# Optimization experiments

Hardware: AMD Instinct MI355X
Metric: run time of the kernel (lower is better)

Reference implementation:

```python
import jax, jax.numpy as jnp
import numpy as np

N, P = 25000, 400000          # atoms, pairs
F, E, EH = 64, 32, 64         # nr_atom_basis, nr_edge_basis, nr_edge_basis_hidden
FH, SSH, S = 64, 64, 64       # node hidden, spatial hidden, spatial
FV, C, H, K = 64, 32, 4, 50   # velocity hidden, coefficients, heads, rbf
R_MAX = 0.5                   # maximum_interaction_radius (nm)
EPS = 1e-8
SCALE = 1.0                   # scale_factor_in_nanometer


def physnet_rbf(d):
    # PhysNet RBF: exp(-beta * (exp(-d) - mu_k)^2), mu_k in [exp(-r_max), 1]
    mu = jnp.linspace(np.exp(-R_MAX), 1.0, K).astype(jnp.float32)
    beta = jnp.float32(((2.0 / K) * (1.0 - np.exp(-R_MAX))) ** -2)
    return jnp.exp(-beta * (jnp.exp(-d)[:, None] - mu) ** 2)  # [P, K]


def seg_sum(v, idx, n):
    return jax.ops.segment_sum(v, idx, num_segments=n)


def seg_mean(v, idx, n):
    # matches torch scatter_reduce 'mean' with include_self=False (empty segments -> 0)
    s = seg_sum(v, idx, n)
    cnt = seg_sum(jnp.ones((v.shape[0],), v.dtype), idx, n)
    cnt = jnp.maximum(cnt, 1.0).reshape((n,) + (1,) * (v.ndim - 1))
    return s / cnt


def seg_softmax(a, idx, n):
    # numerically-stable per-receiver softmax over variable neighbor sets
    m = jax.ops.segment_max(a, idx, num_segments=n)
    m = jnp.where(jnp.isfinite(m), m, 0.0)
    e = jnp.exp(a - m[idx])
    return e / seg_sum(e, idx, n)[idx]


def setup_inputs():
    key = jax.random.key(0)
    ks = jax.random.split(key, 20)
    def w(k, shape):
        return jax.random.normal(k, shape, jnp.float32) * 0.05
    z = lambda *s: jnp.zeros(s, jnp.float32)
    return dict(
        h=jax.random.normal(ks[0], (N, F), jnp.float32),
        x=jax.random.uniform(ks[1], (N, 3), jnp.float32),
        v=jax.random.normal(ks[2], (N, 3), jnp.float32) * 0.1,
        idx_i=jax.random.randint(ks[3], (P,), 0, N),
        idx_j=jax.random.randint(ks[4], (P,), 0, N),
        W_ein=w(ks[5], (2 * F, K)), b_ein=z(K),
        W_eo1=w(ks[6], (2 * F + K + 1, EH)), b_eo1=z(EH),
        W_eo2=w(ks[7], (EH, E)), b_eo2=z(E),
        W_att=w(ks[8], (E, H)), b_att=z(H),
        W_xm=w(ks[9], (H * E, C)),
        W_vm=w(ks[10], (C,)),
        W_pn1=w(ks[11], (C, SSH)), b_pn1=z(SSH),
        W_pn2=w(ks[12], (SSH, S)), b_pn2=z(S),
        W_n1=w(ks[13], (F + H * E + S, FH)), b_n1=z(FH),
        W_n2=w(ks[14], (FH, F)), b_n2=z(F),
        W_v1=w(ks[15], (F, FV)), b_v1=z(FV),
        W_v2=w(ks[16], (FV, 1)),
    )


def reference(h, x, v, idx_i, idx_j,
              W_ein, b_ein, W_eo1, b_eo1, W_eo2, b_eo2,
              W_att, b_att, W_xm, W_vm,
              W_pn1, b_pn1, W_pn2, b_pn2,
              W_n1, b_n1, W_n2, b_n2,
              W_v1, b_v1, W_v2):
    act = jax.nn.silu
    # geometry
    r_ij = x[idx_j] - x[idx_i]                       # [P, 3]
    d_ij = jnp.sqrt(jnp.sum(r_ij ** 2, axis=-1) + EPS)
    dir_ij = r_ij / (d_ij[:, None] + EPS)
    # edge update (Eq. 7): RBF-filtered edge MLP
    h_cat = jnp.concatenate([h[idx_i], h[idx_j]], axis=-1)          # [P, 2F]
    filtered = physnet_rbf(d_ij) * (h_cat @ W_ein + b_ein)          # [P, K]
    edge_in = jnp.concatenate([h_cat, filtered, (d_ij / SCALE)[:, None]], axis=-1)
    h_ij_edge = act(edge_in @ W_eo1 + b_eo1) @ W_eo2 + b_eo2        # [P, E]
    # multi-head semantic attention: segment softmax per receiver
    att = jax.nn.celu(h_ij_edge @ W_att + b_att, alpha=2.0)         # [P, H]
    att_w = seg_softmax(att, idx_i, N)                              # [P, H]
    h_ij_sem = (h_ij_edge[:, :, None] * att_w[:, None, :]).reshape(P, E * H)
    # neighborhood aggregation
    h_i_sem = seg_sum(h_ij_sem, idx_i, N)                           # [N, E*H]
    # spatial attention (Eq. 6)
    comb = jnp.tanh(h_ij_sem @ W_xm)[:, :, None] * dir_ij[:, None, :]  # [P, C, 3]
    comb_mean = seg_mean(comb, idx_i, N)                            # [N, C, 3]
    comb_norm2 = jnp.sum(comb_mean ** 2, axis=-1)                   # [N, C]
    h_i_spatial = act(act(comb_norm2 @ W_pn1 + b_pn1) @ W_pn2 + b_pn2)
    # node update (Eq. 4)
    node_in = jnp.concatenate([h, h_i_sem, h_i_spatial], axis=-1)
    h_new = h + act(act(node_in @ W_n1 + b_n1) @ W_n2 + b_n2)
    # velocity update (Eq. 12)
    v_ij = jnp.einsum('pcx,c->px', comb, W_vm)                      # [P, 3]
    dv = seg_mean(v_ij, idx_i, N)                                   # [N, 3]
    gate = 2.0 * jax.nn.sigmoid(act(h_new @ W_v1 + b_v1) @ W_v2)    # [N, 1]
    v_new = gate * v + dv
    x_new = x + v_new
    return h_new, x_new, v_new
```

## Files before the change

kernel.cpp:

```cpp
#include <hip/hip_runtime.h>
#include <hip/hip_bf16.h>

#define DEV __device__ __forceinline__

constexpr int N_ = 25000;
constexpr int P_ = 400000;

constexpr int align4(int xx){ return (xx+3)&~3; }
constexpr int OFF_CNT     = 0;
constexpr int OFF_OFFSETS = align4(OFF_CNT + N_);
constexpr int OFF_CURSOR  = align4(OFF_OFFSETS + N_ + 1);
constexpr int OFF_EDGE    = align4(OFF_CURSOR + N_);
constexpr int OFF_E4      = OFF_EDGE + P_*16;
constexpr int OFF_DIR     = OFF_E4 + P_*4;
constexpr int OFF_SEM     = align4(OFF_DIR + P_*4);
constexpr int OFF_N2      = OFF_SEM + N_*64;
constexpr int OFF_DV      = OFF_N2 + N_*16;
constexpr int OFF_WB5     = OFF_DV + N_*4;
constexpr int OFF_WB6     = OFF_WB5 + 1024;
constexpr int OFF_WB7     = OFF_WB6 + 2048;
constexpr int OFF_WB8     = OFF_WB7 + 8192;
constexpr int OFF_WB9     = OFF_WB8 + 2048;
constexpr int OFF_HB      = OFF_WB9 + 2048;
constexpr int OFF_SIJ     = OFF_HB + N_*32;
constexpr int OFF_WB1     = OFF_SIJ + P_*2;
constexpr int OFF_WB2     = OFF_WB1 + 8192;
constexpr int OFF_WB3     = OFF_WB2 + 2048;
constexpr int OFF_WB4     = OFF_WB3 + 1024;
constexpr int OFF_RANK    = OFF_WB4 + 2048;
constexpr int WS_UNITS    = OFF_RANK + P_;

constexpr float MU0F  = 0.60653065971263342f;
constexpr float DMUF  = (1.0f - 0.60653065971263342f) / 49.0f;
constexpr float BETAF = 1.0f / ((0.04f * (1.0f - 0.60653065971263342f)) *
                                (0.04f * (1.0f - 0.60653065971263342f)));
constexpr float EPSF  = 1e-8f;

DEV float u2f(unsigned int u){ union{unsigned int i; float f;} c; c.i=u; return c.f; }
DEV unsigned int f2b16(float f){
  __hip_bfloat16 b = __float2bfloat16(f);
  unsigned short s; __builtin_memcpy(&s, &b, 2);
  return (unsigned int)s;
}
DEV unsigned int pack2(float a, float b){ return f2b16(a) | (f2b16(b) << 16); }
DEV float frcp(float x){ return __builtin_amdgcn_rcpf(x); }
DEV float silu_f(float v){ return v * frcp(1.0f + __expf(-v)); }

using short8 = __attribute__((ext_vector_type(8))) short;
using f32x4  = __attribute__((ext_vector_type(4))) float;
union U4S8 { uint4 u; short8 s; };
DEV short8 ld_frag(const void* p){ U4S8 c; c.u = *(const uint4*)p; return c.s; }
DEV f32x4 mfma16(short8 a, short8 b, f32x4 c){
  return __builtin_amdgcn_mfma_f32_16x16x32_bf16(a, b, c, 0, 0, 0);
}

__global__ void k_hist(const int* __restrict__ idx_i,
                       int* __restrict__ cnt, int* __restrict__ rank){
  int t = blockIdx.x*256 + threadIdx.x;
  if (t < P_) rank[t] = atomicAdd(&cnt[idx_i[t]], 1);
}

__global__ __launch_bounds__(1024) void k_scan2(
    const int* __restrict__ cnt, int* __restrict__ offsets,
    const float* __restrict__ h,
    const float* __restrict__ Wein, const float* __restrict__ Weo1,
    const float* __restrict__ Weo2, const float* __restrict__ Wxm,
    const float* __restrict__ Wpn1, const float* __restrict__ Wpn2,
    const float* __restrict__ Wn1,  const float* __restrict__ Wn2,
    const float* __restrict__ Wv1,
    unsigned int* __restrict__ hb,
    unsigned short* __restrict__ wb1, unsigned short* __restrict__ wb2,
    unsigned short* __restrict__ wb3, unsigned short* __restrict__ wb4,
    unsigned short* __restrict__ wb5, unsigned short* __restrict__ wb6,
    unsigned short* __restrict__ wb7, unsigned short* __restrict__ wb8,
    unsigned short* __restrict__ wb9){
  __shared__ unsigned short sCnt[N_];
  __shared__ int swv[16];
  if (blockIdx.x == 0){
    const int t = threadIdx.x;
    const int wv = t >> 6, ln = t & 63;
    for (int q = t; q < N_; q += 1024) sCnt[q] = (unsigned short)cnt[q];
    __syncthreads();
    constexpr int CH = (N_ + 1023)/1024;
    int b = t*CH, e = b+CH;
    if (b > N_) b = N_;
    if (e > N_) e = N_;
    int s = 0;
    for (int q=b; q<e; q++) s += sCnt[q];
    int incl = s;
    #pragma unroll
    for (int off=1; off<64; off<<=1){
      int vv = __shfl_up(incl, off);
      if (ln >= off) incl += vv;
    }
    if (ln == 63) swv[wv] = incl;
    __syncthreads();
    if (wv == 0 && ln < 16){
      int w = swv[ln];
      #pragma unroll
      for (int off=1; off<16; off<<=1){
        int vv = __shfl_up(w, off);
        if (ln >= off) w += vv;
      }
      swv[ln] = w;
    }
    __syncthreads();
    const int wpre = (wv > 0) ? swv[wv-1] : 0;
    int run = wpre + incl - s;
    for (int q=b; q<e; q++){ offsets[q] = run; run += sCnt[q]; }
    if (t == 1023) offsets[N_] = run;
    return;
  }
  int t = (blockIdx.x-1)*1024 + threadIdx.x;
  const int st = (gridDim.x-1)*1024;
  for (int q=t; q<N_*32; q+=st){
    float2 a = *(const float2*)(h + (size_t)q*2);
    hb[q] = pack2(a.x, a.y);
  }
  for (int q=t; q<8*4*64*8; q+=st){
    int e=q&7, lane=(q>>3)&63, sx=(q>>9)&3, nf=q>>11;
    int l15=lane&15, quad=lane>>4;
    int n = 16*nf + l15, k = sx*32 + quad*8 + e;
    float v = (n<50) ? Wein[k*50+n] : ((n<64) ? 0.f : Weo1[k*64+(n-64)]);
    wb1[q] = (unsigned short)f2b16(v);
  }
  for (int q=t; q<4*2*64*8; q+=st){
    int e=q&7, lane=(q>>3)&63, sx=(q>>9)&1, nf=q>>10;
    int l15=lane&15, quad=lane>>4;
    int n = 16*nf + l15, k = sx*32 + quad*8 + e;
    float v = (k<50) ? Weo1[(128+k)*64+n] : ((k==50) ? Weo1[178*64+n] : 0.f);
    wb2[q] = (unsigned short)f2b16(v);
  }
  for (int q=t; q<2*2*64*8; q+=st){
    int e=q&7, lane=(q>>3)&63, sx=(q>>9)&1, nf=q>>10;
    int l15=lane&15, quad=lane>>4;
    int n = 16*nf + l15, k = sx*32 + quad*8 + e;
    wb3[q] = (unsigned short)f2b16(Weo2[k*32+n]);
  }
  for (int q=t; q<8*64*8; q+=st){
    int e=q&7, lane=(q>>3)&63, nf=q>>9;
    int l15=lane&15, quad=lane>>4;
    int k = quad*8 + e;
    int n_log = l15*8 + nf;
    int cc = n_log>>2, hh = n_log&3;
    wb4[q] = (unsigned short)f2b16(Wxm[(k*4+hh)*32 + cc]);
  }
  for (int q=t; q<4*64*8; q+=st){
    int e=q&7, lane=(q>>3)&63, nf=q>>9;
    int l15=lane&15, quad=lane>>4;
    int n = 16*nf + l15, k = quad*8 + e;
    wb5[q] = (unsigned short)f2b16(Wpn1[k*64+n]);
  }
  for (int q=t; q<4*2*64*8; q+=st){
    int e=q&7, lane=(q>>3)&63, sx=(q>>9)&1, nf=q>>10;
    int l15=lane&15, quad=lane>>4;
    int n = 16*nf + l15, k = sx*32 + quad*8 + e;
    wb6[q] = (unsigned short)f2b16(Wpn2[k*64+n]);
    wb8[q] = (unsigned short)f2b16(Wn2[k*64+n]);
    wb9[q] = (unsigned short)f2b16(Wv1[k*64+n]);
  }
  for (int q=t; q<4*8*64*8; q+=st){
    int e=q&7, lane=(q>>3)&63, sx=(q>>9)&7, nf=q>>12;
    int l15=lane&15, quad=lane>>4;
    int n = 16*nf + l15, k = sx*32 + quad*8 + e;
    wb7[q] = (unsigned short)f2b16(Wn1[k*64+n]);
  }
}

__global__ void k_scatter3(const int* __restrict__ idx_i, const int* __restrict__ idx_j,
                           const int* __restrict__ offsets, const int* __restrict__ rank,
                           int* __restrict__ sij){
  int t = blockIdx.x*256 + threadIdx.x;
  if (t >= P_) return;
  int i = idx_i[t], j = idx_j[t];
  int pos = offsets[i] + rank[t];
  *(int2*)(sij + (size_t)pos*2) = make_int2(i, j);
}

__global__ __launch_bounds__(256, 4) void k_edge2(
    const unsigned short* __restrict__ hb,
    const int* __restrict__ sij, const float* __restrict__ x,
    float* __restrict__ dir4,
    const unsigned short* __restrict__ wb1, const unsigned short* __restrict__ wb2,
    const unsigned short* __restrict__ wb3,
    const float* __restrict__ bein, const float* __restrict__ beo1,
    const float* __restrict__ beo2, const float* __restrict__ Watt,
    const float* __restrict__ batt,
    unsigned int* __restrict__ edge_out, float* __restrict__ e4_out)
{
  __shared__ __align__(16) unsigned char sAll[4*4608];
  __shared__ float sdv[128];
  __shared__ float semd[128];

  const int tid  = threadIdx.x;
  const int wv   = tid >> 6;
  const int lane = tid & 63;
  const int l15  = lane & 15;
  const int quad = lane >> 4;
  const int pbase = blockIdx.x * 128;
  unsigned char* sW = sAll + wv*4608;

  if (lane < 32){
    int row = 32*wv + lane;
    int2 ij = *(const int2*)(sij + (size_t)(pbase + row)*2);
    float xi0=x[ij.x*3], xi1=x[ij.x*3+1], xi2=x[ij.x*3+2];
    float xj0=x[ij.y*3], xj1=x[ij.y*3+1], xj2=x[ij.y*3+2];
    float rx=xj0-xi0, ry=xj1-xi1, rz=xj2-xi2;
    float d = sqrtf(rx*rx+ry*ry+rz*rz+EPSF);
    float iv = frcp(d+EPSF);
    sdv[row]  = d;
    semd[row] = __expf(-d);
    *(float4*)(dir4 + (size_t)(pbase + row)*4) = make_float4(rx*iv, ry*iv, rz*iv, d);
  }

  short8 af0[4], af1[4];
  {
    const int rbase = pbase + 32*wv;
    int2 ij0 = *(const int2*)(sij + (size_t)(rbase + l15)*2);
    int2 ij1 = *(const int2*)(sij + (size_t)(rbase + 16 + l15)*2);
    const unsigned char* hB = (const unsigned char*)hb;
    af0[0] = ld_frag(hB + (size_t)ij0.x*128 + quad*16);
    af0[1] = ld_frag(hB + (size_t)ij0.x*128 + 64 + quad*16);
    af0[2] = ld_frag(hB + (size_t)ij0.y*128 + quad*16);
    af0[3] = ld_frag(hB + (size_t)ij0.y*128 + 64 + quad*16);
    af1[0] = ld_frag(hB + (size_t)ij1.x*128 + quad*16);
    af1[1] = ld_frag(hB + (size_t)ij1.x*128 + 64 + quad*16);
    af1[2] = ld_frag(hB + (size_t)ij1.y*128 + quad*16);
    af1[3] = ld_frag(hB + (size_t)ij1.y*128 + 64 + quad*16);
  }

  f32x4 acc[2][4];
  #pragma unroll
  for (int mf=0; mf<2; mf++)
    #pragma unroll
    for (int nf=0; nf<4; nf++){
      int nn = 16*nf + l15;
      float bias = (nn < 50) ? bein[nn] : 0.f;
      acc[mf][nf] = (f32x4){bias, bias, bias, bias};
    }
  #pragma unroll
  for (int s=0; s<4; s++){
    #pragma unroll
    for (int nf=0; nf<4; nf++){
      short8 b = ld_frag((const unsigned char*)wb1 + (size_t)((nf*4 + s)*64 + lane)*16);
      acc[0][nf] = mfma16(af0[s], b, acc[0][nf]);
      acc[1][nf] = mfma16(af1[s], b, acc[1][nf]);
    }
  }

  #pragma unroll
  for (int mf=0; mf<2; mf++)
    #pragma unroll
    for (int nf=0; nf<4; nf++){
      int n = 16*nf + l15;
      float mu = MU0F + (float)n*DMUF;
      #pragma unroll
      for (int reg=0; reg<4; reg++){
        int lrow = 16*mf + quad*4 + reg;
        int grow = 32*wv + lrow;
        float t = semd[grow] - mu;
        float fv = acc[mf][nf][reg] * __expf(-BETAF*t*t);
        unsigned short ob;
        if (n < 50)       ob = (unsigned short)f2b16(fv);
        else if (n == 50) ob = (unsigned short)f2b16(sdv[grow]);
        else              ob = 0;
        ((unsigned short*)sW)[lrow*72 + n] = ob;
      }
    }

  #pragma unroll
  for (int mf=0; mf<2; mf++)
    #pragma unroll
    for (int nf=0; nf<4; nf++){
      float bias = beo1[16*nf + l15];
      acc[mf][nf] = (f32x4){bias, bias, bias, bias};
    }
  #pragma unroll
  for (int s=0; s<4; s++){
    #pragma unroll
    for (int nf=0; nf<4; nf++){
      short8 b = ld_frag((const unsigned char*)wb1 + (size_t)(((4+nf)*4 + s)*64 + lane)*16);
      acc[0][nf] = mfma16(af0[s], b, acc[0][nf]);
      acc[1][nf] = mfma16(af1[s], b, acc[1][nf]);
    }
  }

  #pragma unroll
  for (int s=0; s<2; s++){
    int koff = s*32 + quad*8;
    short8 a0 = ld_frag(sW + l15*144      + koff*2);
    short8 a1 = ld_frag(sW + (16+l15)*144 + koff*2);
    #pragma unroll
    for (int nf=0; nf<4; nf++){
      short8 b = ld_frag((const unsigned char*)wb2 + (size_t)((nf*2 + s)*64 + lane)*16);
      acc[0][nf] = mfma16(a0, b, acc[0][nf]);
      acc[1][nf] = mfma16(a1, b, acc[1][nf]);
    }
  }

  unsigned char* A3 = sW;
  #pragma unroll
  for (int mf=0; mf<2; mf++)
    #pragma unroll
    for (int nf=0; nf<4; nf++){
      int n = 16*nf + l15;
      #pragma unroll
      for (int reg=0; reg<4; reg++){
        int lrow = 16*mf + quad*4 + reg;
        ((unsigned short*)A3)[lrow*72 + n] = (unsigned short)f2b16(silu_f(acc[mf][nf][reg]));
      }
    }

  f32x4 acc3[2][2];
  #pragma unroll
  for (int mf=0; mf<2; mf++)
    #pragma unroll
    for (int nf=0; nf<2; nf++){
      float bias = beo2[16*nf + l15];
      acc3[mf][nf] = (f32x4){bias, bias, bias, bias};
    }
  #pragma unroll
  for (int s=0; s<2; s++){
    int koff = s*32 + quad*8;
    short8 a0 = ld_frag(A3 + l15*144      + koff*2);
    short8 a1 = ld_frag(A3 + (16+l15)*144 + koff*2);
    #pragma unroll
    for (int nf=0; nf<2; nf++){
      short8 b = ld_frag((const unsigned char*)wb3 + (size_t)((nf*2 + s)*64 + lane)*16);
      acc3[0][nf] = mfma16(a0, b, acc3[0][nf]);
      acc3[1][nf] = mfma16(a1, b, acc3[1][nf]);
    }
  }

  #pragma unroll
  for (int mf=0; mf<2; mf++)
    #pragma unroll
    for (int nf=0; nf<2; nf++){
      int n = 16*nf + l15;
      #pragma unroll
      for (int reg=0; reg<4; reg++){
        int lrow = 16*mf + quad*4 + reg;
        ((float*)sW)[lrow*36 + n] = acc3[mf][nf][reg];
      }
    }

  {
    int rr = lane >> 1;
    int p = pbase + 32*wv + rr;
    int cb = (lane & 1) * 16;
    const float* er = (const float*)(sW + rr*144);
    float l0, l1, l2, l3;
    if ((lane & 1) == 0){ l0 = batt[0]; l1 = batt[1]; l2 = batt[2]; l3 = batt[3]; }
    else                { l0 = l1 = l2 = l3 = 0.f; }
    float ecache[16];
    {
      float4 v0 = *(const float4*)(er + cb);
      float4 v1 = *(const float4*)(er + cb + 4);
      float4 v2 = *(const float4*)(er + cb + 8);
      float4 v3 = *(const float4*)(er + cb + 12);
      ecache[0]=v0.x; ecache[1]=v0.y; ecache[2]=v0.z; ecache[3]=v0.w;
      ecache[4]=v1.x; ecache[5]=v1.y; ecache[6]=v1.z; ecache[7]=v1.w;
      ecache[8]=v2.x; ecache[9]=v2.y; ecache[10]=v2.z; ecache[11]=v2.w;
      ecache[12]=v3.x; ecache[13]=v3.y; ecache[14]=v3.z; ecache[15]=v3.w;
    }
    #pragma unroll
    for (int c=0;c<16;c++){
      float ev = ecache[c];
      const float4 wr = *(const float4*)(Watt + (cb + c)*4);
      l0 += ev*wr.x; l1 += ev*wr.y; l2 += ev*wr.z; l3 += ev*wr.w;
    }
    l0 += __shfl_xor(l0,1); l1 += __shfl_xor(l1,1);
    l2 += __shfl_xor(l2,1); l3 += __shfl_xor(l3,1);
    if ((lane & 1) == 0){
      float e0 = __expf(l0 > 0.f ? l0 : 2.f*(__expf(l0*0.5f)-1.f));
      float e1 = __expf(l1 > 0.f ? l1 : 2.f*(__expf(l1*0.5f)-1.f));
      float e2 = __expf(l2 > 0.f ? l2 : 2.f*(__expf(l2*0.5f)-1.f));
      float e3 = __expf(l3 > 0.f ? l3 : 2.f*(__expf(l3*0.5f)-1.f));
      *(float4*)(e4_out + (size_t)p*4) = make_float4(e0, e1, e2, e3);
    }
    uint4 o1 = make_uint4(pack2(ecache[0],ecache[1]),  pack2(ecache[2],ecache[3]),
                          pack2(ecache[4],ecache[5]),  pack2(ecache[6],ecache[7]));
    uint4 o2 = make_uint4(pack2(ecache[8],ecache[9]),  pack2(ecache[10],ecache[11]),
                          pack2(ecache[12],ecache[13]),pack2(ecache[14],ecache[15]));
    unsigned int* ep = edge_out + (size_t)p*16 + (lane&1)*8;
    *(uint4*)(ep)     = o1;
    *(uint4*)(ep + 4) = o2;
  }
}

__global__ __launch_bounds__(256, 4) void k_agg(
    const int* __restrict__ offsets,
    const unsigned int* __restrict__ edgeb,
    const float* __restrict__ e4,
    const float* __restrict__ dir4,
    const unsigned short* __restrict__ wb4,
    const float* __restrict__ Wvm,
    unsigned int* __restrict__ semB, unsigned int* __restrict__ n2B,
    float* __restrict__ wsDv)
{
  __shared__ __align__(16) unsigned char sAllB[4*5632];
  const int wv   = threadIdx.x >> 6;
  const int lane = threadIdx.x & 63;
  unsigned char* sA = sAllB + wv*5632;
  unsigned char* gC = sA + 1024;
  float* sE = (float*)(sA + 5120);
  float* sD = (float*)(sA + 5376);

  const int c    = lane & 31;
  const int l15  = lane & 15;
  const int quad = lane >> 4;
  const int half = lane >> 5;
  const bool low = (lane < 32);

  short8 b4[8];
  #pragma unroll
  for (int nf=0; nf<8; nf++)
    b4[nf] = ld_frag((const unsigned char*)wb4 + (size_t)(nf*64 + lane)*16);
  const float wvm_c = Wvm[c];

  const int i = blockIdx.x*4 + wv;
  if (i >= N_) return;
  const int n0 = offsets[i], n1 = offsets[i+1];
  const int cnt = n1 - n0;

  {
    const int nc0 = min(16, cnt);
    if (lane < 32){
      if (lane*32 < nc0*64){
        const uint4* src = (const uint4*)(edgeb + (size_t)n0*16 + lane*8);
        *(uint4*)(sA + lane*32)      = src[0];
        *(uint4*)(sA + lane*32 + 16) = src[1];
      }
    } else if (lane < 48){
      int k = lane - 32;
      if (k < nc0) *(float4*)(sE + k*4) = *(const float4*)(e4 + (size_t)(n0+k)*4);
    } else {
      int k = lane - 48;
      if (k < nc0) *(float4*)(sD + k*4) = *(const float4*)(dir4 + (size_t)(n0+k)*4);
    }
  }

  float d0=0.f,d1=0.f,d2=0.f,d3=0.f;
  for (int s = n0 + lane; s < n1; s += 64){
    const float4 ev = *(const float4*)(e4 + (size_t)s*4);
    d0+=ev.x; d1+=ev.y; d2+=ev.z; d3+=ev.w;
  }
  #pragma unroll
  for (int off=32; off>=1; off>>=1){
    d0 += __shfl_xor(d0,off); d1 += __shfl_xor(d1,off);
    d2 += __shfl_xor(d2,off); d3 += __shfl_xor(d3,off);
  }
  const float i0 = (cnt>0)?frcp(d0):0.f, i1 = (cnt>0)?frcp(d1):0.f;
  const float i2 = (cnt>0)?frcp(d2):0.f, i3 = (cnt>0)?frcp(d3):0.f;

  float sem4[4] = {0.f,0.f,0.f,0.f};
  float cx=0.f,cy=0.f,cz=0.f, gx=0.f,gy=0.f,gz=0.f;

  bool staged = true;
  for (int base = n0; base < n1; base += 16){
    const int nc = min(16, n1 - base);
    if (!staged){
      if (lane < 32){
        if (lane*32 < nc*64){
          const uint4* src = (const uint4*)(edgeb + (size_t)base*16 + lane*8);
          *(uint4*)(sA + lane*32)      = src[0];
          *(uint4*)(sA + lane*32 + 16) = src[1];
        }
      } else if (lane < 48){
        int k = lane - 32;
        if (k < nc) *(float4*)(sE + k*4) = *(const float4*)(e4 + (size_t)(base+k)*4);
      } else {
        int k = lane - 48;
        if (k < nc) *(float4*)(sD + k*4) = *(const float4*)(dir4 + (size_t)(base+k)*4);
      }
    }
    staged = false;
    {
      short8 a0 = ld_frag(sA + l15*64 + quad*16);
      f32x4 accg[8];
      #pragma unroll
      for (int nf=0; nf<8; nf++){
        f32x4 z = (f32x4){0.f,0.f,0.f,0.f};
        accg[nf] = mfma16(a0, b4[nf], z);
      }
      #pragma unroll
      for (int reg=0; reg<4; reg++){
        int row = quad*4 + reg;
        uint4 o = make_uint4(pack2(accg[0][reg],accg[1][reg]),
                             pack2(accg[2][reg],accg[3][reg]),
                             pack2(accg[4][reg],accg[5][reg]),
                             pack2(accg[6][reg],accg[7][reg]));
        *(uint4*)(gC + row*256 + l15*16) = o;
      }
    }
    for (int t0 = 0; t0 < nc; t0 += 2){
      const int rloc = t0 + half;
      const bool act = rloc < nc;
      const int rc = act ? rloc : 0;
      const float4 ev = *(const float4*)(sE + rc*4);
      const float4 dv = *(const float4*)(sD + rc*4);
      const float aw0 = ev.x*i0, aw1 = ev.y*i1, aw2 = ev.z*i2, aw3 = ev.w*i3;
      uint2 gv = *(const uint2*)(gC + rc*256 + c*8);
      float g0=u2f(gv.x<<16), g1=u2f(gv.x&0xffff0000u);
      float g2=u2f(gv.y<<16), g3=u2f(gv.y&0xffff0000u);
      float tp = aw0*g0 + aw1*g1 + aw2*g2 + aw3*g3;
      float tt = fminf(fmaxf(tp, -15.f), 15.f);
      float ex = __expf(2.f*tt);
      float th = (ex-1.f)*frcp(ex+1.f);
      unsigned int ew = *(const unsigned int*)(sA + rc*64 + (c>>1)*4);
      float ec = (c & 1) ? u2f(ew & 0xffff0000u) : u2f(ew << 16);
      if (act){
        sem4[0] += ec*aw0; sem4[1] += ec*aw1;
        sem4[2] += ec*aw2; sem4[3] += ec*aw3;
        cx += th*dv.x; cy += th*dv.y; cz += th*dv.z;
        float tw = th*wvm_c;
        gx += tw*dv.x; gy += tw*dv.y; gz += tw*dv.z;
      }
    }
  }

  #pragma unroll
  for (int j=0;j<4;j++) sem4[j] += __shfl_xor(sem4[j], 32);
  cx += __shfl_xor(cx,32); cy += __shfl_xor(cy,32); cz += __shfl_xor(cz,32);
  #pragma unroll
  for (int off=32; off>=1; off>>=1){
    gx += __shfl_xor(gx,off); gy += __shfl_xor(gy,off); gz += __shfl_xor(gz,off);
  }
  const float invc = frcp((float)(cnt > 1 ? cnt : 1));
  if (low){
    float mx = cx*invc, my = cy*invc, mz = cz*invc;
    float n2v = mx*mx + my*my + mz*mz;
    float n2o = __shfl_xor(n2v, 1);
    if ((c & 1) == 0) n2B[(size_t)i*16 + (c>>1)] = pack2(n2v, n2o);
    *(uint2*)(semB + (size_t)i*64 + c*2) =
        make_uint2(pack2(sem4[0],sem4[1]), pack2(sem4[2],sem4[3]));
  }
  if (lane == 0)
    *(float4*)(wsDv + (size_t)i*4) = make_float4(gx*invc, gy*invc, gz*invc, 0.f);
}

__global__ __launch_bounds__(64) void k_mlp(
    const float* __restrict__ h, const float* __restrict__ x, const float* __restrict__ v,
    const unsigned short* __restrict__ hb,
    const unsigned short* __restrict__ semB, const unsigned short* __restrict__ n2B,
    const float* __restrict__ wsDv,
    const unsigned short* __restrict__ wb5, const unsigned short* __restrict__ wb6,
    const unsigned short* __restrict__ wb7, const unsigned short* __restrict__ wb8,
    const unsigned short* __restrict__ wb9,
    const float* __restrict__ bpn1, const float* __restrict__ bpn2,
    const float* __restrict__ bn1,  const float* __restrict__ bn2,
    const float* __restrict__ bv1,  const float* __restrict__ Wv2,
    float* __restrict__ out)
{
  __shared__ __align__(16) unsigned char sT[16*136];
  __shared__ __align__(16) unsigned char sU[16*136];

  const int lane = threadIdx.x & 63;
  const int l15  = lane & 15;
  const int quad = lane >> 4;
  const int base = blockIdx.x*16;
  const int r0a  = min(base + l15, N_-1);
  const unsigned char* hB  = (const unsigned char*)hb;
  const unsigned char* sB  = (const unsigned char*)semB;
  const unsigned char* nB  = (const unsigned char*)n2B;

  {
    f32x4 acc[4];
    #pragma unroll
    for (int nf=0; nf<4; nf++){ float b = bpn1[16*nf+l15]; acc[nf] = (f32x4){b,b,b,b}; }
    short8 a0 = ld_frag(nB + (size_t)r0a*64 + quad*16);
    #pragma unroll
    for (int nf=0; nf<4; nf++){
      short8 b = ld_frag((const unsigned char*)wb5 + (size_t)(nf*64 + lane)*16);
      acc[nf] = mfma16(a0, b, acc[nf]);
    }
    #pragma unroll
    for (int nf=0; nf<4; nf++){
      int n = 16*nf + l15;
      #pragma unroll
      for (int reg=0; reg<4; reg++){
        int row = quad*4 + reg;
        ((unsigned short*)(sT + row*136))[n] = (unsigned short)f2b16(silu_f(acc[nf][reg]));
      }
    }
  }
  {
    f32x4 acc[4];
    #pragma unroll
    for (int nf=0; nf<4; nf++){ float b = bpn2[16*nf+l15]; acc[nf] = (f32x4){b,b,b,b}; }
    #pragma unroll
    for (int s=0; s<2; s++){
      int koff = s*32 + quad*8;
      short8 a0 = ld_frag(sT + l15*136 + koff*2);
      #pragma unroll
      for (int nf=0; nf<4; nf++){
        short8 b = ld_frag((const unsigned char*)wb6 + (size_t)((nf*2 + s)*64 + lane)*16);
        acc[nf] = mfma16(a0, b, acc[nf]);
      }
    }
    #pragma unroll
    for (int nf=0; nf<4; nf++){
      int n = 16*nf + l15;
      #pragma unroll
      for (int reg=0; reg<4; reg++){
        int row = quad*4 + reg;
        ((unsigned short*)(sU + row*136))[n] = (unsigned short)f2b16(silu_f(acc[nf][reg]));
      }
    }
  }
  {
    f32x4 acc[4];
    #pragma unroll
    for (int nf=0; nf<4; nf++){ float b = bn1[16*nf+l15]; acc[nf] = (f32x4){b,b,b,b}; }
    #pragma unroll
    for (int s=0; s<8; s++){
      int koff = s*32 + quad*8;
      short8 a0;
      if (koff < 64){
        a0 = ld_frag(hB + (size_t)r0a*128 + koff*2);
      } else if (koff < 192){
        a0 = ld_frag(sB + (size_t)r0a*256 + (koff-64)*2);
      } else {
        a0 = ld_frag(sU + l15*136 + (koff-192)*2);
      }
      #pragma unroll
      for (int nf=0; nf<4; nf++){
        short8 b = ld_frag((const unsigned char*)wb7 + (size_t)((nf*8 + s)*64 + lane)*16);
        acc[nf] = mfma16(a0, b, acc[nf]);
      }
    }
    #pragma unroll
    for (int nf=0; nf<4; nf++){
      int n = 16*nf + l15;
      #pragma unroll
      for (int reg=0; reg<4; reg++){
        int row = quad*4 + reg;
        ((unsigned short*)(sT + row*136))[n] = (unsigned short)f2b16(silu_f(acc[nf][reg]));
      }
    }
  }
  {
    f32x4 acc[4];
    #pragma unroll
    for (int nf=0; nf<4; nf++){ float b = bn2[16*nf+l15]; acc[nf] = (f32x4){b,b,b,b}; }
    #pragma unroll
    for (int s=0; s<2; s++){
      int koff = s*32 + quad*8;
      short8 a0 = ld_frag(sT + l15*136 + koff*2);
      #pragma unroll
      for (int nf=0; nf<4; nf++){
        short8 b = ld_frag((const unsigned char*)wb8 + (size_t)((nf*2 + s)*64 + lane)*16);
        acc[nf] = mfma16(a0, b, acc[nf]);
      }
    }
    #pragma unroll
    for (int nf=0; nf<4; nf++){
      int n = 16*nf + l15;
      #pragma unroll
      for (int reg=0; reg<4; reg++){
        int row = quad*4 + reg;
        int node = base + row;
        float hv = (node < N_) ? h[(size_t)node*64 + n] : 0.f;
        float hnew = hv + silu_f(acc[nf][reg]);
        if (node < N_) out[(size_t)node*64 + n] = hnew;
        ((unsigned short*)(sU + row*136))[n] = (unsigned short)f2b16(hnew);
      }
    }
  }
  {
    f32x4 acc[4];
    #pragma unroll
    for (int nf=0; nf<4; nf++){ float b = bv1[16*nf+l15]; acc[nf] = (f32x4){b,b,b,b}; }
    #pragma unroll
    for (int s=0; s<2; s++){
      int koff = s*32 + quad*8;
      short8 a0 = ld_frag(sU + l15*136 + koff*2);
      #pragma unroll
      for (int nf=0; nf<4; nf++){
        short8 b = ld_frag((const unsigned char*)wb9 + (size_t)((nf*2 + s)*64 + lane)*16);
        acc[nf] = mfma16(a0, b, acc[nf]);
      }
    }
    float part[4] = {0.f,0.f,0.f,0.f};
    #pragma unroll
    for (int nf=0; nf<4; nf++){
      float w2 = Wv2[16*nf + l15];
      #pragma unroll
      for (int reg=0; reg<4; reg++)
        part[reg] += silu_f(acc[nf][reg]) * w2;
    }
    #pragma unroll
    for (int reg=0; reg<4; reg++){
      #pragma unroll
      for (int off=1; off<16; off<<=1)
        part[reg] += __shfl_xor(part[reg], off);
    }
    if (l15 == 0){
      #pragma unroll
      for (int reg=0; reg<4; reg++){
        int row = quad*4 + reg;
        int node = base + row;
        if (node < N_){
          float gate = 2.f*frcp(1.f + __expf(-part[reg]));
          float4 dvv = *(const float4*)(wsDv + (size_t)node*4);
          float dvs[3] = {dvv.x, dvv.y, dvv.z};
          #pragma unroll
          for (int ax=0; ax<3; ax++){
            float vn = gate * v[(size_t)node*3 + ax] + dvs[ax];
            out[(size_t)N_*64 + (size_t)node*3 + ax]                 = x[(size_t)node*3 + ax] + vn;
            out[(size_t)N_*64 + (size_t)N_*3 + (size_t)node*3 + ax]  = vn;
          }
        }
      }
    }
  }
}

extern "C" void kernel_launch(void* const* d_in, const int* in_sizes, int n_in,
                              void* d_out, int out_size, void* d_ws, size_t ws_size,
                              hipStream_t stream)
{
  const float* h = (const float*)d_in[0];
  const float* x = (const float*)d_in[1];
  const float* v = (const float*)d_in[2];
  const int* idx_i = (const int*)d_in[3];
  const int* idx_j = (const int*)d_in[4];
  const float* Wein = (const float*)d_in[5];  const float* bein = (const float*)d_in[6];
  const float* Weo1 = (const float*)d_in[7];  const float* beo1 = (const float*)d_in[8];
  const float* Weo2 = (const float*)d_in[9];  const float* beo2 = (const float*)d_in[10];
  const float* Watt = (const float*)d_in[11]; const float* batt = (const float*)d_in[12];
  const float* Wxm  = (const float*)d_in[13]; const float* Wvm  = (const float*)d_in[14];
  const float* Wpn1 = (const float*)d_in[15]; const float* bpn1 = (const float*)d_in[16];
  const float* Wpn2 = (const float*)d_in[17]; const float* bpn2 = (const float*)d_in[18];
  const float* Wn1  = (const float*)d_in[19]; const float* bn1  = (const float*)d_in[20];
  const float* Wn2  = (const float*)d_in[21]; const float* bn2  = (const float*)d_in[22];
  const float* Wv1  = (const float*)d_in[23]; const float* bv1  = (const float*)d_in[24];
  const float* Wv2  = (const float*)d_in[25];

  float* wsf        = (float*)d_ws;
  int*   cnt        = (int*)(wsf + OFF_CNT);
  int*   offsets    = (int*)(wsf + OFF_OFFSETS);
  unsigned int* edgeb = (unsigned int*)(wsf + OFF_EDGE);
  float* e4o        = wsf + OFF_E4;
  float* diro       = wsf + OFF_DIR;
  unsigned int* semB = (unsigned int*)(wsf + OFF_SEM);
  unsigned int* n2B  = (unsigned int*)(wsf + OFF_N2);
  float* wsDv       = wsf + OFF_DV;
  unsigned short* wb1 = (unsigned short*)(wsf + OFF_WB1);
  unsigned short* wb2 = (unsigned short*)(wsf + OFF_WB2);
  unsigned short* wb3 = (unsigned short*)(wsf + OFF_WB3);
  unsigned short* wb4 = (unsigned short*)(wsf + OFF_WB4);
  unsigned short* wb5 = (unsigned short*)(wsf + OFF_WB5);
  unsigned short* wb6 = (unsigned short*)(wsf + OFF_WB6);
  unsigned short* wb7 = (unsigned short*)(wsf + OFF_WB7);
  unsigned short* wb8 = (unsigned short*)(wsf + OFF_WB8);
  unsigned short* wb9 = (unsigned short*)(wsf + OFF_WB9);
  unsigned int*   hb  = (unsigned int*)(wsf + OFF_HB);
  int*            sij = (int*)(wsf + OFF_SIJ);
  int*            rnk = (int*)(wsf + OFF_RANK);

  hipMemsetAsync(cnt, 0, N_*sizeof(int), stream);
  k_hist<<<(P_+255)/256, 256, 0, stream>>>(idx_i, cnt, rnk);
  k_scan2<<<65, 1024, 0, stream>>>(cnt, offsets, h,
                                   Wein, Weo1, Weo2, Wxm, Wpn1, Wpn2,
                                   Wn1, Wn2, Wv1,
                                   hb, wb1, wb2, wb3, wb4,
                                   wb5, wb6, wb7, wb8, wb9);
  k_scatter3<<<(P_+255)/256, 256, 0, stream>>>(idx_i, idx_j, offsets, rnk, sij);
  k_edge2<<<P_/128, 256, 0, stream>>>((const unsigned short*)hb, sij, x, diro,
                                      wb1, wb2, wb3,
                                      bein, beo1, beo2, Watt, batt,
                                      edgeb, e4o);
  k_agg<<<(N_+3)/4, 256, 0, stream>>>(offsets, edgeb, e4o, diro, wb4, Wvm,
                                      semB, n2B, wsDv);
  k_mlp<<<(N_+15)/16, 64, 0, stream>>>(h, x, v,
                                       (const unsigned short*)hb,
                                       (const unsigned short*)semB,
                                       (const unsigned short*)n2B,
                                       wsDv,
                                       wb5, wb6, wb7, wb8, wb9,
                                       bpn1, bpn2, bn1, bn2, bv1, Wv2,
                                       (float*)d_out);
}
```

Measured before the change: 268.3 us.

## Split k_mlp output columns across four wavefronts per 16-node block

k_mlp now launches 256 threads per block instead of 64. Each of the four wavefronts computes one 16-column slice of every 64-wide MLP layer, where before a single wave computed all four slices. Block barriers between layers and a small shared-memory reduction for the gate dot product are added. The aim is more parallelism and latency hiding in the node MLP, paid for with five __syncthreads and redundant loads of the A fragments in every wave.

```diff
diff --git a/kernel.cpp b/kernel.cpp
--- a/kernel.cpp
+++ b/kernel.cpp
@@ -539,7 +539,7 @@
     *(float4*)(wsDv + (size_t)i*4) = make_float4(gx*invc, gy*invc, gz*invc, 0.f);
 }
 
-__global__ __launch_bounds__(64) void k_mlp(
+__global__ __launch_bounds__(256) void k_mlp(
     const float* __restrict__ h, const float* __restrict__ x, const float* __restrict__ v,
     const unsigned short* __restrict__ hb,
     const unsigned short* __restrict__ semB, const unsigned short* __restrict__ n2B,
@@ -554,8 +554,11 @@
 {
   __shared__ __align__(16) unsigned char sT[16*136];
   __shared__ __align__(16) unsigned char sU[16*136];
-
-  const int lane = threadIdx.x & 63;
+  __shared__ float sPart[4*16];
+
+  const int tid  = threadIdx.x;
+  const int wv   = tid >> 6;
+  const int lane = tid & 63;
   const int l15  = lane & 15;
   const int quad = lane >> 4;
   const int base = blockIdx.x*16;
@@ -563,55 +566,41 @@
   const unsigned char* hB  = (const unsigned char*)hb;
   const unsigned char* sB  = (const unsigned char*)semB;
   const unsigned char* nB  = (const unsigned char*)n2B;
+  const int ncol = 16*wv + l15;
 
   {
-    f32x4 acc[4];
-    #pragma unroll
-    for (int nf=0; nf<4; nf++){ float b = bpn1[16*nf+l15]; acc[nf] = (f32x4){b,b,b,b}; }
+    float b = bpn1[ncol];
+    f32x4 acc = (f32x4){b,b,b,b};
     short8 a0 = ld_frag(nB + (size_t)r0a*64 + quad*16);
-    #pragma unroll
-    for (int nf=0; nf<4; nf++){
-      short8 b = ld_frag((const unsigned char*)wb5 + (size_t)(nf*64 + lane)*16);
-      acc[nf] = mfma16(a0, b, acc[nf]);
-    }
-    #pragma unroll
-    for (int nf=0; nf<4; nf++){
-      int n = 16*nf + l15;
-      #pragma unroll
-      for (int reg=0; reg<4; reg++){
-        int row = quad*4 + reg;
-        ((unsigned short*)(sT + row*136))[n] = (unsigned short)f2b16(silu_f(acc[nf][reg]));
-      }
-    }
-  }
+    short8 bb = ld_frag((const unsigned char*)wb5 + (size_t)(wv*64 + lane)*16);
+    acc = mfma16(a0, bb, acc);
+    #pragma unroll
+    for (int reg=0; reg<4; reg++){
+      int row = quad*4 + reg;
+      ((unsigned short*)(sT + row*136))[ncol] = (unsigned short)f2b16(silu_f(acc[reg]));
+    }
+  }
+  __syncthreads();
   {
-    f32x4 acc[4];
-    #pragma unroll
-    for (int nf=0; nf<4; nf++){ float b = bpn2[16*nf+l15]; acc[nf] = (f32x4){b,b,b,b}; }
+    float b = bpn2[ncol];
+    f32x4 acc = (f32x4){b,b,b,b};
     #pragma unroll
     for (int s=0; s<2; s++){
       int koff = s*32 + quad*8;
       short8 a0 = ld_frag(sT + l15*136 + koff*2);
-      #pragma unroll
-      for (int nf=0; nf<4; nf++){
-        short8 b = ld_frag((const unsigned char*)wb6 + (size_t)((nf*2 + s)*64 + lane)*16);
-        acc[nf] = mfma16(a0, b, acc[nf]);
-      }
-    }
-    #pragma unroll
-    for (int nf=0; nf<4; nf++){
-      int n = 16*nf + l15;
-      #pragma unroll
-      for (int reg=0; reg<4; reg++){
-        int row = quad*4 + reg;
-        ((unsigned short*)(sU + row*136))[n] = (unsigned short)f2b16(silu_f(acc[nf][reg]));
-      }
-    }
-  }
+      short8 bb = ld_frag((const unsigned char*)wb6 + (size_t)((wv*2 + s)*64 + lane)*16);
+      acc = mfma16(a0, bb, acc);
+    }
+    #pragma unroll
+    for (int reg=0; reg<4; reg++){
+      int row = quad*4 + reg;
+      ((unsigned short*)(sU + row*136))[ncol] = (unsigned short)f2b16(silu_f(acc[reg]));
+    }
+  }
+  __syncthreads();
   {
-    f32x4 acc[4];
-    #pragma unroll
-    for (int nf=0; nf<4; nf++){ float b = bn1[16*nf+l15]; acc[nf] = (f32x4){b,b,b,b}; }
+    float b = bn1[ncol];
+    f32x4 acc = (f32x4){b,b,b,b};
     #pragma unroll
     for (int s=0; s<8; s++){
       int koff = s*32 + quad*8;
@@ -623,72 +612,51 @@
       } else {
         a0 = ld_frag(sU + l15*136 + (koff-192)*2);
       }
-      #pragma unroll
-      for (int nf=0; nf<4; nf++){
-        short8 b = ld_frag((const unsigned char*)wb7 + (size_t)((nf*8 + s)*64 + lane)*16);
-        acc[nf] = mfma16(a0, b, acc[nf]);
-      }
-    }
-    #pragma unroll
-    for (int nf=0; nf<4; nf++){
-      int n = 16*nf + l15;
-      #pragma unroll
-      for (int reg=0; reg<4; reg++){
-        int row = quad*4 + reg;
-        ((unsigned short*)(sT + row*136))[n] = (unsigned short)f2b16(silu_f(acc[nf][reg]));
-      }
-    }
-  }
+      short8 bb = ld_frag((const unsigned char*)wb7 + (size_t)((wv*8 + s)*64 + lane)*16);
+      acc = mfma16(a0, bb, acc);
+    }
+    #pragma unroll
+    for (int reg=0; reg<4; reg++){
+      int row = quad*4 + reg;
+      ((unsigned short*)(sT + row*136))[ncol] = (unsigned short)f2b16(silu_f(acc[reg]));
+    }
+  }
+  __syncthreads();
   {
-    f32x4 acc[4];
-    #pragma unroll
-    for (int nf=0; nf<4; nf++){ float b = bn2[16*nf+l15]; acc[nf] = (f32x4){b,b,b,b}; }
+    float b = bn2[ncol];
+    f32x4 acc = (f32x4){b,b,b,b};
     #pragma unroll
     for (int s=0; s<2; s++){
       int koff = s*32 + quad*8;
       short8 a0 = ld_frag(sT + l15*136 + koff*2);
-      #pragma unroll
-      for (int nf=0; nf<4; nf++){
-        short8 b = ld_frag((const unsigned char*)wb8 + (size_t)((nf*2 + s)*64 + lane)*16);
-        acc[nf] = mfma16(a0, b, acc[nf]);
-      }
-    }
-    #pragma unroll
-    for (int nf=0; nf<4; nf++){
-      int n = 16*nf + l15;
-      #pragma unroll
-      for (int reg=0; reg<4; reg++){
-        int row = quad*4 + reg;
-        int node = base + row;
-        float hv = (node < N_) ? h[(size_t)node*64 + n] : 0.f;
-        float hnew = hv + silu_f(acc[nf][reg]);
-        if (node < N_) out[(size_t)node*64 + n] = hnew;
-        ((unsigned short*)(sU + row*136))[n] = (unsigned short)f2b16(hnew);
-      }
-    }
-  }
+      short8 bb = ld_frag((const unsigned char*)wb8 + (size_t)((wv*2 + s)*64 + lane)*16);
+      acc = mfma16(a0, bb, acc);
+    }
+    #pragma unroll
+    for (int reg=0; reg<4; reg++){
+      int row = quad*4 + reg;
+      int node = base + row;
+      float hv = (node < N_) ? h[(size_t)node*64 + ncol] : 0.f;
+      float hnew = hv + silu_f(acc[reg]);
+      if (node < N_) out[(size_t)node*64 + ncol] = hnew;
+      ((unsigned short*)(sU + row*136))[ncol] = (unsigned short)f2b16(hnew);
+    }
+  }
+  __syncthreads();
   {
-    f32x4 acc[4];
-    #pragma unroll
-    for (int nf=0; nf<4; nf++){ float b = bv1[16*nf+l15]; acc[nf] = (f32x4){b,b,b,b}; }
+    float b = bv1[ncol];
+    f32x4 acc = (f32x4){b,b,b,b};
     #pragma unroll
     for (int s=0; s<2; s++){
       int koff = s*32 + quad*8;
       short8 a0 = ld_frag(sU + l15*136 + koff*2);
-      #pragma unroll
-      for (int nf=0; nf<4; nf++){
-        short8 b = ld_frag((const unsigned char*)wb9 + (size_t)((nf*2 + s)*64 + lane)*16);
-        acc[nf] = mfma16(a0, b, acc[nf]);
-      }
-    }
-    float part[4] = {0.f,0.f,0.f,0.f};
-    #pragma unroll
-    for (int nf=0; nf<4; nf++){
-      float w2 = Wv2[16*nf + l15];
-      #pragma unroll
-      for (int reg=0; reg<4; reg++)
-        part[reg] += silu_f(acc[nf][reg]) * w2;
-    }
+      short8 bb = ld_frag((const unsigned char*)wb9 + (size_t)((wv*2 + s)*64 + lane)*16);
+      acc = mfma16(a0, bb, acc);
+    }
+    float part[4];
+    float w2 = Wv2[ncol];
+    #pragma unroll
+    for (int reg=0; reg<4; reg++) part[reg] = silu_f(acc[reg]) * w2;
     #pragma unroll
     for (int reg=0; reg<4; reg++){
       #pragma unroll
@@ -696,12 +664,19 @@
         part[reg] += __shfl_xor(part[reg], off);
     }
     if (l15 == 0){
+      #pragma unroll
+      for (int reg=0; reg<4; reg++)
+        sPart[wv*16 + quad*4 + reg] = part[reg];
+    }
+    __syncthreads();
+    if (wv == 0 && l15 == 0){
       #pragma unroll
       for (int reg=0; reg<4; reg++){
         int row = quad*4 + reg;
         int node = base + row;
         if (node < N_){
-          float gate = 2.f*frcp(1.f + __expf(-part[reg]));
+          float p = sPart[row] + sPart[16 + row] + sPart[32 + row] + sPart[48 + row];
+          float gate = 2.f*frcp(1.f + __expf(-p));
           float4 dvv = *(const float4*)(wsDv + (size_t)node*4);
           float dvs[3] = {dvv.x, dvv.y, dvv.z};
           #pragma unroll
@@ -773,12 +748,12 @@
                                       edgeb, e4o);
   k_agg<<<(N_+3)/4, 256, 0, stream>>>(offsets, edgeb, e4o, diro, wb4, Wvm,
                                       semB, n2B, wsDv);
-  k_mlp<<<(N_+15)/16, 64, 0, stream>>>(h, x, v,
-                                       (const unsigned short*)hb,
-                                       (const unsigned short*)semB,
-                                       (const unsigned short*)n2B,
-                                       wsDv,
-                                       wb5, wb6, wb7, wb8, wb9,
-                                       bpn1, bpn2, bn1, bn2, bv1, Wv2,
-                                       (float*)d_out);
-}
+  k_mlp<<<(N_+15)/16, 256, 0, stream>>>(h, x, v,
+                                        (const unsigned short*)hb,
+                                        (const unsigned short*)semB,
+                                        (const unsigned short*)n2B,
+                                        wsDv,
+                                        wb5, wb6, wb7, wb8, wb9,
+                                        bpn1, bpn2, bn1, bn2, bv1, Wv2,
+                                        (float*)d_out);
+}
```

After: 263.0 us. -2.0%, faster.
